# Kernel optimization log

Measured on AMD Instinct MI355X. Metric: run time of the kernel, lower is better.

The kernel has to match this reference:

```python
import jax, jax.numpy as jnp
import numpy as np

B, T, D, H = 128, 512, 16, 512


def lstm_layer(x, h0, c0, Wih, Whh, b):
    """Single LSTM layer, batch_first input x: (B,T,Din). Torch gate order i,f,g,o.
    b is the sum of torch's b_ih + b_hh (identical math)."""
    def step(carry, xt):
        h, c = carry
        gates = xt @ Wih.T + h @ Whh.T + b  # (B, 4H)
        i, f, g, o = jnp.split(gates, 4, axis=-1)
        i = jax.nn.sigmoid(i)
        f = jax.nn.sigmoid(f)
        g = jnp.tanh(g)
        o = jax.nn.sigmoid(o)
        c = f * c + i * g
        h = o * jnp.tanh(c)
        return (h, c), h

    (hT, cT), ys = jax.lax.scan(step, (h0, c0), jnp.swapaxes(x, 0, 1))
    return jnp.swapaxes(ys, 0, 1), hT, cT  # (B,T,H), (B,H), (B,H)


def setup_inputs() -> dict:
    key = jax.random.key(0)
    ks = jax.random.split(key, 16)
    s = 1.0 / np.sqrt(H)  # torch LSTM/Linear init scale
    u = lambda k, shape: jax.random.uniform(k, shape, jnp.float32, -s, s)
    return {
        "x": jax.random.normal(ks[0], (B, T, D), jnp.float32),
        # encoder layer 0: input_dim -> H ; layer 1: H -> H
        "enc_Wih0": u(ks[1], (4 * H, D)),
        "enc_Whh0": u(ks[2], (4 * H, H)),
        "enc_b0": u(ks[3], (4 * H,)),
        "enc_Wih1": u(ks[4], (4 * H, H)),
        "enc_Whh1": u(ks[5], (4 * H, H)),
        "enc_b1": u(ks[6], (4 * H,)),
        # decoder layers: H -> H
        "dec_Wih0": u(ks[7], (4 * H, H)),
        "dec_Whh0": u(ks[8], (4 * H, H)),
        "dec_b0": u(ks[9], (4 * H,)),
        "dec_Wih1": u(ks[10], (4 * H, H)),
        "dec_Whh1": u(ks[11], (4 * H, H)),
        "dec_b1": u(ks[12], (4 * H,)),
        # output projection H -> D
        "W_out": u(ks[13], (D, H)),
        "b_out": u(ks[14], (D,)),
    }


def reference(x, enc_Wih0, enc_Whh0, enc_b0, enc_Wih1, enc_Whh1, enc_b1,
              dec_Wih0, dec_Whh0, dec_b0, dec_Wih1, dec_Whh1, dec_b1,
              W_out, b_out):
    z = jnp.zeros((x.shape[0], H), x.dtype)
    # encoder (2 stacked layers, eval mode -> no dropout)
    y0, h0, c0 = lstm_layer(x, z, z, enc_Wih0, enc_Whh0, enc_b0)
    y1, h1, c1 = lstm_layer(y0, z, z, enc_Wih1, enc_Whh1, enc_b1)
    encoding = h1  # h_n[-1]
    # decoder input: encoding repeated across time
    dec_in = jnp.broadcast_to(encoding[:, None, :], (x.shape[0], x.shape[1], H))
    # decoder initial state = encoder final (h_n, c_n), per-layer
    d0, _, _ = lstm_layer(dec_in, h0, c0, dec_Wih0, dec_Whh0, dec_b0)
    d1, _, _ = lstm_layer(d0, h1, c1, dec_Wih1, dec_Whh1, dec_b1)
    reconstructed = d1 @ W_out.T + b_out  # (B,T,D)
    return reconstructed, encoding
```

## Files before the change

kernel.cpp:

```cpp
#include <hip/hip_runtime.h>
#include <math.h>


#define NB 128
#define NT 512
#define ND 16
#define NH 512
#define NWG 256
#define NTHR 256
#define NGRP 8
#define GWG 32

typedef __attribute__((ext_vector_type(8))) short short8;
typedef __attribute__((ext_vector_type(4))) float float4v;
typedef __attribute__((ext_vector_type(4))) unsigned int uint4v;

#define SCOPE_AGT __HIP_MEMORY_SCOPE_AGENT
#define SCOPE_WG  __HIP_MEMORY_SCOPE_WORKGROUP

#define BAR_BYTES 16384
#define PLANE_BYTES (NB * NH * 4)
#define CHUNK_BYTES (32 * NB * 4)
#define AH_PLANE(wsB, L, par) ((wsB) + BAR_BYTES + (size_t)((L) * 2 + (par)) * PLANE_BYTES)
#define H3F_PTR(wsB, par) ((float*)((wsB) + BAR_BYTES + 8 * (size_t)PLANE_BYTES + (size_t)(par) * NB * NH * 4))

__device__ __forceinline__ void st_u32_agt(unsigned* p, unsigned v) {
  __hip_atomic_store(p, v, __ATOMIC_RELAXED, SCOPE_AGT);
}
__device__ __forceinline__ unsigned ld_u32_agt(const unsigned* p) {
  return __hip_atomic_load(p, __ATOMIC_RELAXED, SCOPE_AGT);
}
__device__ __forceinline__ unsigned long long ld_u64_agt(const void* p) {
  return __hip_atomic_load((const unsigned long long*)p, __ATOMIC_RELAXED, SCOPE_AGT);
}

__device__ __forceinline__ void loadpair(bool fast, const char* pa, const char* pb,
                                         uint4v (&d)[4]) {
  if (fast) {
    asm volatile(
        "global_load_dwordx4 %0, %4, off sc0\n\t"
        "global_load_dwordx4 %1, %4, off offset:16 sc0\n\t"
        "global_load_dwordx4 %2, %5, off sc0\n\t"
        "global_load_dwordx4 %3, %5, off offset:16 sc0\n\t"
        "s_waitcnt vmcnt(0)"
        : "=&v"(d[0]), "=&v"(d[1]), "=&v"(d[2]), "=&v"(d[3])
        : "v"(pa), "v"(pb)
        : "memory");
  } else {
#pragma unroll
    for (int r = 0; r < 2; ++r) {
      const char* base = r ? pb : pa;
      unsigned long long q0 = ld_u64_agt(base);
      unsigned long long q1 = ld_u64_agt(base + 8);
      unsigned long long q2 = ld_u64_agt(base + 16);
      unsigned long long q3 = ld_u64_agt(base + 24);
      d[2 * r][0] = (unsigned)q0; d[2 * r][1] = (unsigned)(q0 >> 32);
      d[2 * r][2] = (unsigned)q1; d[2 * r][3] = (unsigned)(q1 >> 32);
      d[2 * r + 1][0] = (unsigned)q2; d[2 * r + 1][1] = (unsigned)(q2 >> 32);
      d[2 * r + 1][2] = (unsigned)q3; d[2 * r + 1][3] = (unsigned)(q3 >> 32);
    }
  }
}

__device__ __forceinline__ void gbar(unsigned* flags, int hb, unsigned& epoch) {
  ++epoch;
  __syncthreads();
  if (threadIdx.x < 64) {
    if (threadIdx.x == 0) st_u32_agt(flags + hb, epoch);
    const unsigned* fp = flags + (threadIdx.x & 31);
    for (;;) {
      unsigned v = ld_u32_agt(fp);
      if (__all((int)(v - epoch) >= 0)) break;
      __builtin_amdgcn_s_sleep(1);
    }
  }
  __syncthreads();
}

__device__ __forceinline__ unsigned short f2bf(float f) {
  union { float f; unsigned u; } v; v.f = f;
  unsigned r = v.u + 0x7fffu + ((v.u >> 16) & 1u);
  return (unsigned short)(r >> 16);
}
__device__ __forceinline__ float bf2f(unsigned short u) {
  union { float f; unsigned u; } v; v.u = ((unsigned)u) << 16; return v.f;
}
__device__ __forceinline__ void split2(float f, unsigned short& hi, unsigned short& lo) {
  hi = f2bf(f);
  lo = f2bf(f - bf2f(hi));
}
__device__ __forceinline__ void load_wfrag(const float* __restrict__ p, short8& h, short8& l) {
#pragma unroll
  for (int j = 0; j < 8; ++j) {
    unsigned short a, b2; split2(p[j], a, b2);
    h[j] = (short)a; l[j] = (short)b2;
  }
}
__device__ __forceinline__ void load_frags_single(const float* __restrict__ W, int w, int hb, int lane,
                                                  short8 (&fh)[4][4], short8 (&fl)[4][4]) {
  const int ln = lane & 15, lq = lane >> 4;
#pragma unroll
  for (int cc = 0; cc < 4; ++cc) {
    const int k = (w * 4 + cc) * 32 + lq * 8;
#pragma unroll
    for (int g = 0; g < 4; ++g)
      load_wfrag(W + (size_t)(g * NH + hb * 16 + ln) * NH + k, fh[cc][g], fl[cc][g]);
  }
}
__device__ __forceinline__ void load_frags_concat(const float* __restrict__ Wa, const float* __restrict__ Wb,
                                                  int w, int hb, int lane,
                                                  short8 (&fh)[8][4], short8 (&fl)[8][4]) {
  const int ln = lane & 15, lq = lane >> 4;
#pragma unroll
  for (int cc = 0; cc < 8; ++cc) {
    const int k = (w * 8 + cc) * 32 + lq * 8;
    const float* W = (k < 512) ? Wa : Wb;
    const int kk = (k < 512) ? k : k - 512;
#pragma unroll
    for (int g = 0; g < 4; ++g)
      load_wfrag(W + (size_t)(g * NH + hb * 16 + ln) * NH + kk, fh[cc][g], fl[cc][g]);
  }
}

__device__ __forceinline__ void consume2(const uint4v& a, const uint4v& b,
                                         const short8 (&wh)[4], const short8 (&wl)[4],
                                         float4v (&acc)[4]) {
  unsigned x0 = a[0], x1 = a[1], x2 = a[2], x3 = a[3];
  unsigned x4 = b[0], x5 = b[1], x6 = b[2], x7 = b[3];
  union U { unsigned u[4]; short8 s; } A, L;
  A.u[0] = (x0 & 0xffffu) | (x1 << 16);
  A.u[1] = (x2 & 0xffffu) | (x3 << 16);
  A.u[2] = (x4 & 0xffffu) | (x5 << 16);
  A.u[3] = (x6 & 0xffffu) | (x7 << 16);
  L.u[0] = (x0 >> 16) | (x1 & 0xffff0000u);
  L.u[1] = (x2 >> 16) | (x3 & 0xffff0000u);
  L.u[2] = (x4 >> 16) | (x5 & 0xffff0000u);
  L.u[3] = (x6 >> 16) | (x7 & 0xffff0000u);
  const short8 ah = A.s, al = L.s;
#pragma unroll
  for (int g = 0; g < 4; ++g) {
    acc[g] = __builtin_amdgcn_mfma_f32_16x16x32_bf16(ah, wh[g], acc[g], 0, 0, 0);
    acc[g] = __builtin_amdgcn_mfma_f32_16x16x32_bf16(ah, wl[g], acc[g], 0, 0, 0);
    acc[g] = __builtin_amdgcn_mfma_f32_16x16x32_bf16(al, wh[g], acc[g], 0, 0, 0);
  }
}
__device__ __forceinline__ void write_red(float* __restrict__ red, int w, int lane, const float4v (&acc)[4]) {
  const int ln = lane & 15, lq = lane >> 4;
#pragma unroll
  for (int g = 0; g < 4; ++g)
#pragma unroll
    for (int r = 0; r < 4; ++r)
      red[((w * 4 + g) * 16 + (lq * 4 + r)) * 16 + ln] = acc[g][r];
}
__device__ __forceinline__ void store_h(bool fast, char* __restrict__ plane, int b, int hid, float h) {
  unsigned short hi, lo; split2(h, hi, lo);
  const size_t off = (size_t)(hid >> 5) * CHUNK_BYTES + (size_t)b * 128 + (size_t)(hid & 31) * 4;
  unsigned* p = (unsigned*)(plane + off);
  unsigned v = (unsigned)hi | ((unsigned)lo << 16);
  if (fast) __hip_atomic_store(p, v, __ATOMIC_RELAXED, SCOPE_WG);
  else      st_u32_agt(p, v);
}
__device__ __forceinline__ void st_f32s(bool fast, float* p, float v) {
  if (fast) __hip_atomic_store(p, v, __ATOMIC_RELAXED, SCOPE_WG);
  else      __hip_atomic_store(p, v, __ATOMIC_RELAXED, SCOPE_AGT);
}
__device__ __forceinline__ float sigf(float v) { return 1.f / (1.f + __expf(-v)); }

extern "C" __global__ __launch_bounds__(NTHR, 1)
void lstm_ae_kernel(const float* __restrict__ x,
                    const float* __restrict__ eWih0, const float* __restrict__ eWhh0, const float* __restrict__ eb0,
                    const float* __restrict__ eWih1, const float* __restrict__ eWhh1, const float* __restrict__ eb1,
                    const float* __restrict__ dWih0, const float* __restrict__ dWhh0, const float* __restrict__ db0,
                    const float* __restrict__ dWih1, const float* __restrict__ dWhh1, const float* __restrict__ db1,
                    const float* __restrict__ Wout,  const float* __restrict__ bout,
                    float* __restrict__ out, char* __restrict__ wsB) {
  __shared__ float red0[4 * 4 * 16 * 16];
  __shared__ float red1[4 * 4 * 16 * 16];
  __shared__ unsigned sh_slot;

  unsigned* xcnt   = (unsigned*)(wsB + 9216);
  unsigned* gflags = (unsigned*)(wsB + 10240);

  const int tid = threadIdx.x;
  const int lane = tid & 63;
  const int w = tid >> 6;

  const unsigned xcc = (unsigned)__builtin_amdgcn_s_getreg(63508) & 15u;
  if (tid == 0)
    sh_slot = __hip_atomic_fetch_add(xcnt + (xcc & 7u), 1u, __ATOMIC_RELAXED, SCOPE_AGT);
  __syncthreads();
  const unsigned slot = sh_slot;
  if (tid == 0) st_u32_agt(gflags + blockIdx.x, 1u);
  if (tid < 64) {
    for (;;) {
      int ok = 1;
#pragma unroll
      for (int j = 0; j < 4; ++j) ok &= (ld_u32_agt(gflags + lane * 4 + j) != 0u);
      if (__all(ok)) break;
      __builtin_amdgcn_s_sleep(1);
    }
  }
  __syncthreads();
  bool good = (slot < GWG);
#pragma unroll
  for (int k = 0; k < 8; ++k) good = good && (ld_u32_agt(xcnt + k) == GWG);

  const int grp = good ? (int)(xcc & 7u) : (blockIdx.x & 7);
  const int hb  = good ? (int)slot        : (blockIdx.x >> 3);
  const bool fast = good;

  unsigned* flags = (unsigned*)(wsB + (size_t)grp * 1024);
  unsigned epoch = 0;

  const int b0 = grp * 16;
  const int ln = lane & 15, lq = lane >> 4;
  const int aoff = (b0 + ln) * 128 + lq * 32;
  const int bi = tid >> 4, hi_ = tid & 15;
  const int b = b0 + bi, hid = hb * 16 + hi_;
  const float4v zacc = {0.f, 0.f, 0.f, 0.f};

  store_h(fast, AH_PLANE(wsB, 0, 1), b, hid, 0.f);
  store_h(fast, AH_PLANE(wsB, 1, 1), b, hid, 0.f);
  float c0 = 0.f, c1 = 0.f, c2 = 0.f, c3 = 0.f;
  const float eb0v[4] = {eb0[hid], eb0[NH + hid], eb0[2 * NH + hid], eb0[3 * NH + hid]};
  const float eb1v[4] = {eb1[hid], eb1[NH + hid], eb1[2 * NH + hid], eb1[3 * NH + hid]};
  const float db1v[4] = {db1[hid], db1[NH + hid], db1[2 * NH + hid], db1[3 * NH + hid]};

  short8 w0h[4][4], w0l[4][4];
  short8 w1h[8][4], w1l[8][4];
  load_frags_single(eWhh0, w, hb, lane, w0h, w0l);
  load_frags_concat(eWih1, eWhh1, w, hb, lane, w1h, w1l);
  gbar(flags, hb, epoch);

  float h0fin = 0.f, h1fin = 0.f;

  for (int i = 0; i <= NT; ++i) {
    const int pw = i & 1, pr = pw ^ 1;
    const int te = i - 1;
    const int pA = te & 1, pB = pA ^ 1;
    const char* p0 = AH_PLANE(wsB, 0, pr);
    const char* p1 = (w < 2) ? AH_PLANE(wsB, 0, pA) : AH_PLANE(wsB, 1, pB);
    const int c1i = (w < 2) ? w * 8 : (w - 2) * 8;
    float4v acc0[4] = {zacc, zacc, zacc, zacc};
    float4v acc1[4] = {zacc, zacc, zacc, zacc};
    uint4v d[4];

    loadpair(fast, p0 + (size_t)(w * 4 + 0) * CHUNK_BYTES + aoff,
                   p0 + (size_t)(w * 4 + 1) * CHUNK_BYTES + aoff, d);
    consume2(d[0], d[1], w0h[0], w0l[0], acc0);
    consume2(d[2], d[3], w0h[1], w0l[1], acc0);
    loadpair(fast, p0 + (size_t)(w * 4 + 2) * CHUNK_BYTES + aoff,
                   p0 + (size_t)(w * 4 + 3) * CHUNK_BYTES + aoff, d);
    consume2(d[0], d[1], w0h[2], w0l[2], acc0);
    consume2(d[2], d[3], w0h[3], w0l[3], acc0);
    write_red(red0, w, lane, acc0);
#pragma unroll
    for (int pp = 0; pp < 4; ++pp) {
      loadpair(fast, p1 + (size_t)(c1i + 2 * pp) * CHUNK_BYTES + aoff,
                     p1 + (size_t)(c1i + 2 * pp + 1) * CHUNK_BYTES + aoff, d);
      consume2(d[0], d[1], w1h[2 * pp], w1l[2 * pp], acc1);
      consume2(d[2], d[3], w1h[2 * pp + 1], w1l[2 * pp + 1], acc1);
    }
    write_red(red1, w, lane, acc1);
    __syncthreads();

    if (i < NT) {
      float s[4];
#pragma unroll
      for (int g = 0; g < 4; ++g) {
        float v = eb0v[g];
#pragma unroll
        for (int ww = 0; ww < 4; ++ww) v += red0[((ww * 4 + g) * 16 + bi) * 16 + hi_];
        s[g] = v;
      }
      const float* xr = x + ((size_t)b * NT + i) * ND;
      float xv[16];
#pragma unroll
      for (int j = 0; j < 16; ++j) xv[j] = xr[j];
#pragma unroll
      for (int g = 0; g < 4; ++g) {
        const float* wr = eWih0 + (size_t)(g * NH + hid) * ND;
        float v = 0.f;
#pragma unroll
        for (int j = 0; j < 16; ++j) v += xv[j] * wr[j];
        s[g] += v;
      }
      float ig = sigf(s[0]), fg = sigf(s[1]), gg = tanhf(s[2]), og = sigf(s[3]);
      c0 = fg * c0 + ig * gg;
      float h = og * tanhf(c0);
      store_h(fast, AH_PLANE(wsB, 0, pw), b, hid, h);
      if (i == NT - 1) h0fin = h;
    }
    if (i >= 1) {
      float s[4];
#pragma unroll
      for (int g = 0; g < 4; ++g) {
        float v = eb1v[g];
#pragma unroll
        for (int ww = 0; ww < 4; ++ww) v += red1[((ww * 4 + g) * 16 + bi) * 16 + hi_];
        s[g] = v;
      }
      float ig = sigf(s[0]), fg = sigf(s[1]), gg = tanhf(s[2]), og = sigf(s[3]);
      c1 = fg * c1 + ig * gg;
      float h = og * tanhf(c1);
      store_h(fast, AH_PLANE(wsB, 1, pA), b, hid, h);
      if (te == NT - 1) h1fin = h;
    }
    gbar(flags, hb, epoch);
  }

  out[(size_t)NB * NT * ND + (size_t)b * NH + hid] = h1fin;
  c2 = c0; c3 = c1;
  store_h(fast, AH_PLANE(wsB, 2, 1), b, hid, h0fin);
  store_h(fast, AH_PLANE(wsB, 3, 1), b, hid, h1fin);

  float Gbreg[4];
  load_frags_single(dWih0, w, hb, lane, w0h, w0l);
  {
    const char* ph = AH_PLANE(wsB, 1, 1);
    float4v acc[4] = {zacc, zacc, zacc, zacc};
    uint4v d[4];
    loadpair(fast, ph + (size_t)(w * 4 + 0) * CHUNK_BYTES + aoff,
                   ph + (size_t)(w * 4 + 1) * CHUNK_BYTES + aoff, d);
    consume2(d[0], d[1], w0h[0], w0l[0], acc);
    consume2(d[2], d[3], w0h[1], w0l[1], acc);
    loadpair(fast, ph + (size_t)(w * 4 + 2) * CHUNK_BYTES + aoff,
                   ph + (size_t)(w * 4 + 3) * CHUNK_BYTES + aoff, d);
    consume2(d[0], d[1], w0h[2], w0l[2], acc);
    consume2(d[2], d[3], w0h[3], w0l[3], acc);
    write_red(red0, w, lane, acc);
    __syncthreads();
#pragma unroll
    for (int g = 0; g < 4; ++g) {
      float v = db0[g * NH + hid];
#pragma unroll
      for (int ww = 0; ww < 4; ++ww) v += red0[((ww * 4 + g) * 16 + bi) * 16 + hi_];
      Gbreg[g] = v;
    }
  }
  load_frags_single(dWhh0, w, hb, lane, w0h, w0l);
  load_frags_concat(dWih1, dWhh1, w, hb, lane, w1h, w1l);
  gbar(flags, hb, epoch);

  const int idxA = hb * 8 + w * 2, idxB = idxA + 1;
  const int pbA = b0 + (idxA >> 4), pdA = idxA & 15;
  const int pbB = b0 + (idxB >> 4), pdB = idxB & 15;

  for (int i = 0; i <= NT + 1; ++i) {
    const int pw = i & 1, pr = pw ^ 1;
    const int te = i - 1, tp = i - 2;
    const int pA = te & 1, pB = pA ^ 1;
    const char* p0 = AH_PLANE(wsB, 2, pr);
    const char* p1 = (w < 2) ? AH_PLANE(wsB, 2, pA) : AH_PLANE(wsB, 3, pB);
    const int c1i = (w < 2) ? w * 8 : (w - 2) * 8;
    const float* H3 = H3F_PTR(wsB, tp & 1);
    float4v acc0[4] = {zacc, zacc, zacc, zacc};
    float4v acc1[4] = {zacc, zacc, zacc, zacc};
    uint4v d[4];

    loadpair(fast, p0 + (size_t)(w * 4 + 0) * CHUNK_BYTES + aoff,
                   p0 + (size_t)(w * 4 + 1) * CHUNK_BYTES + aoff, d);
    consume2(d[0], d[1], w0h[0], w0l[0], acc0);
    consume2(d[2], d[3], w0h[1], w0l[1], acc0);
    loadpair(fast, p0 + (size_t)(w * 4 + 2) * CHUNK_BYTES + aoff,
                   p0 + (size_t)(w * 4 + 3) * CHUNK_BYTES + aoff, d);
    consume2(d[0], d[1], w0h[2], w0l[2], acc0);
    consume2(d[2], d[3], w0h[3], w0l[3], acc0);
    write_red(red0, w, lane, acc0);
#pragma unroll
    for (int pp = 0; pp < 4; ++pp) {
      loadpair(fast, p1 + (size_t)(c1i + 2 * pp) * CHUNK_BYTES + aoff,
                     p1 + (size_t)(c1i + 2 * pp + 1) * CHUNK_BYTES + aoff, d);
      consume2(d[0], d[1], w1h[2 * pp], w1l[2 * pp], acc1);
      consume2(d[2], d[3], w1h[2 * pp + 1], w1l[2 * pp + 1], acc1);
    }
    write_red(red1, w, lane, acc1);
    uint4v dp[4];
    loadpair(fast, (const char*)(H3 + (size_t)pbA * NH) + (size_t)lane * 32,
                   (const char*)(H3 + (size_t)pbB * NH) + (size_t)lane * 32, dp);
    __syncthreads();

    if (i >= 2) {
#pragma unroll
      for (int rep = 0; rep < 2; ++rep) {
        union PU { uint4v u; float f[4]; } u0, u1;
        u0.u = dp[2 * rep]; u1.u = dp[2 * rep + 1];
        const int pd = rep ? pdB : pdA;
        const float* wr = Wout + (size_t)pd * NH + lane * 8;
        float ssum = u0.f[0] * wr[0] + u0.f[1] * wr[1] + u0.f[2] * wr[2] + u0.f[3] * wr[3]
                   + u1.f[0] * wr[4] + u1.f[1] * wr[5] + u1.f[2] * wr[6] + u1.f[3] * wr[7];
#pragma unroll
        for (int off = 32; off >= 1; off >>= 1) ssum += __shfl_xor(ssum, off, 64);
        if (lane == 0)
          out[((size_t)(rep ? pbB : pbA) * NT + tp) * ND + pd] = ssum + bout[pd];
      }
    }
    if (i < NT) {
      float s[4];
#pragma unroll
      for (int g = 0; g < 4; ++g) {
        float v = Gbreg[g];
#pragma unroll
        for (int ww = 0; ww < 4; ++ww) v += red0[((ww * 4 + g) * 16 + bi) * 16 + hi_];
        s[g] = v;
      }
      float ig = sigf(s[0]), fg = sigf(s[1]), gg = tanhf(s[2]), og = sigf(s[3]);
      c2 = fg * c2 + ig * gg;
      float h = og * tanhf(c2);
      store_h(fast, AH_PLANE(wsB, 2, pw), b, hid, h);
    }
    if (i >= 1 && i <= NT) {
      float s[4];
#pragma unroll
      for (int g = 0; g < 4; ++g) {
        float v = db1v[g];
#pragma unroll
        for (int ww = 0; ww < 4; ++ww) v += red1[((ww * 4 + g) * 16 + bi) * 16 + hi_];
        s[g] = v;
      }
      float ig = sigf(s[0]), fg = sigf(s[1]), gg = tanhf(s[2]), og = sigf(s[3]);
      c3 = fg * c3 + ig * gg;
      float h = og * tanhf(c3);
      store_h(fast, AH_PLANE(wsB, 3, pA), b, hid, h);
      st_f32s(fast, H3F_PTR(wsB, pA) + (size_t)b * NH + hid, h);
    }
    if (i != NT + 1) gbar(flags, hb, epoch);
  }
}

extern "C" void kernel_launch(void* const* d_in, const int* in_sizes, int n_in,
                              void* d_out, int out_size, void* d_ws, size_t ws_size,
                              hipStream_t stream) {
  const float* xp    = (const float*)d_in[0];
  const float* eWih0 = (const float*)d_in[1];
  const float* eWhh0 = (const float*)d_in[2];
  const float* eb0   = (const float*)d_in[3];
  const float* eWih1 = (const float*)d_in[4];
  const float* eWhh1 = (const float*)d_in[5];
  const float* eb1   = (const float*)d_in[6];
  const float* dWih0 = (const float*)d_in[7];
  const float* dWhh0 = (const float*)d_in[8];
  const float* db0   = (const float*)d_in[9];
  const float* dWih1 = (const float*)d_in[10];
  const float* dWhh1 = (const float*)d_in[11];
  const float* db1   = (const float*)d_in[12];
  const float* Wout  = (const float*)d_in[13];
  const float* bout  = (const float*)d_in[14];

  hipMemsetAsync(d_ws, 0, BAR_BYTES, stream);
  lstm_ae_kernel<<<NWG, NTHR, 0, stream>>>(
      xp, eWih0, eWhh0, eb0, eWih1, eWhh1, eb1,
      dWih0, dWhh0, db0, dWih1, dWhh1, db1, Wout, bout,
      (float*)d_out, (char*)d_ws);
}
```

Before: 9.032 ms.

## Drop XCC-aware group placement and use uniform agent-scope loads/stores

Measured after the change: 9.218 ms. 1.02x slower.

```diff
diff --git a/kernel.cpp b/kernel.cpp
--- a/kernel.cpp
+++ b/kernel.cpp
@@ -16,7 +16,6 @@
 typedef __attribute__((ext_vector_type(4))) unsigned int uint4v;
 
 #define SCOPE_AGT __HIP_MEMORY_SCOPE_AGENT
-#define SCOPE_WG  __HIP_MEMORY_SCOPE_WORKGROUP
 
 #define BAR_BYTES 16384
 #define PLANE_BYTES (NB * NH * 4)
@@ -30,36 +29,18 @@
 __device__ __forceinline__ unsigned ld_u32_agt(const unsigned* p) {
   return __hip_atomic_load(p, __ATOMIC_RELAXED, SCOPE_AGT);
 }
-__device__ __forceinline__ unsigned long long ld_u64_agt(const void* p) {
-  return __hip_atomic_load((const unsigned long long*)p, __ATOMIC_RELAXED, SCOPE_AGT);
-}
-
-__device__ __forceinline__ void loadpair(bool fast, const char* pa, const char* pb,
+
+__device__ __forceinline__ void loadpair(const char* pa, const char* pb,
                                          uint4v (&d)[4]) {
-  if (fast) {
-    asm volatile(
-        "global_load_dwordx4 %0, %4, off sc0\n\t"
-        "global_load_dwordx4 %1, %4, off offset:16 sc0\n\t"
-        "global_load_dwordx4 %2, %5, off sc0\n\t"
-        "global_load_dwordx4 %3, %5, off offset:16 sc0\n\t"
-        "s_waitcnt vmcnt(0)"
-        : "=&v"(d[0]), "=&v"(d[1]), "=&v"(d[2]), "=&v"(d[3])
-        : "v"(pa), "v"(pb)
-        : "memory");
-  } else {
-#pragma unroll
-    for (int r = 0; r < 2; ++r) {
-      const char* base = r ? pb : pa;
-      unsigned long long q0 = ld_u64_agt(base);
-      unsigned long long q1 = ld_u64_agt(base + 8);
-      unsigned long long q2 = ld_u64_agt(base + 16);
-      unsigned long long q3 = ld_u64_agt(base + 24);
-      d[2 * r][0] = (unsigned)q0; d[2 * r][1] = (unsigned)(q0 >> 32);
-      d[2 * r][2] = (unsigned)q1; d[2 * r][3] = (unsigned)(q1 >> 32);
-      d[2 * r + 1][0] = (unsigned)q2; d[2 * r + 1][1] = (unsigned)(q2 >> 32);
-      d[2 * r + 1][2] = (unsigned)q3; d[2 * r + 1][3] = (unsigned)(q3 >> 32);
-    }
-  }
+  asm volatile(
+      "global_load_dwordx4 %0, %4, off sc1\n\t"
+      "global_load_dwordx4 %1, %4, off offset:16 sc1\n\t"
+      "global_load_dwordx4 %2, %5, off sc1\n\t"
+      "global_load_dwordx4 %3, %5, off offset:16 sc1\n\t"
+      "s_waitcnt vmcnt(0)"
+      : "=&v"(d[0]), "=&v"(d[1]), "=&v"(d[2]), "=&v"(d[3])
+      : "v"(pa), "v"(pb)
+      : "memory");
 }
 
 __device__ __forceinline__ void gbar(unsigned* flags, int hb, unsigned& epoch) {
@@ -152,17 +133,11 @@
     for (int r = 0; r < 4; ++r)
       red[((w * 4 + g) * 16 + (lq * 4 + r)) * 16 + ln] = acc[g][r];
 }
-__device__ __forceinline__ void store_h(bool fast, char* __restrict__ plane, int b, int hid, float h) {
+__device__ __forceinline__ void store_h(char* __restrict__ plane, int b, int hid, float h) {
   unsigned short hi, lo; split2(h, hi, lo);
   const size_t off = (size_t)(hid >> 5) * CHUNK_BYTES + (size_t)b * 128 + (size_t)(hid & 31) * 4;
-  unsigned* p = (unsigned*)(plane + off);
   unsigned v = (unsigned)hi | ((unsigned)lo << 16);
-  if (fast) __hip_atomic_store(p, v, __ATOMIC_RELAXED, SCOPE_WG);
-  else      st_u32_agt(p, v);
-}
-__device__ __forceinline__ void st_f32s(bool fast, float* p, float v) {
-  if (fast) __hip_atomic_store(p, v, __ATOMIC_RELAXED, SCOPE_WG);
-  else      __hip_atomic_store(p, v, __ATOMIC_RELAXED, SCOPE_AGT);
+  st_u32_agt((unsigned*)(plane + off), v);
 }
 __device__ __forceinline__ float sigf(float v) { return 1.f / (1.f + __expf(-v)); }
 
@@ -176,38 +151,13 @@
                     float* __restrict__ out, char* __restrict__ wsB) {
   __shared__ float red0[4 * 4 * 16 * 16];
   __shared__ float red1[4 * 4 * 16 * 16];
-  __shared__ unsigned sh_slot;
-
-  unsigned* xcnt   = (unsigned*)(wsB + 9216);
-  unsigned* gflags = (unsigned*)(wsB + 10240);
 
   const int tid = threadIdx.x;
   const int lane = tid & 63;
   const int w = tid >> 6;
 
-  const unsigned xcc = (unsigned)__builtin_amdgcn_s_getreg(63508) & 15u;
-  if (tid == 0)
-    sh_slot = __hip_atomic_fetch_add(xcnt + (xcc & 7u), 1u, __ATOMIC_RELAXED, SCOPE_AGT);
-  __syncthreads();
-  const unsigned slot = sh_slot;
-  if (tid == 0) st_u32_agt(gflags + blockIdx.x, 1u);
-  if (tid < 64) {
-    for (;;) {
-      int ok = 1;
-#pragma unroll
-      for (int j = 0; j < 4; ++j) ok &= (ld_u32_agt(gflags + lane * 4 + j) != 0u);
-      if (__all(ok)) break;
-      __builtin_amdgcn_s_sleep(1);
-    }
-  }
-  __syncthreads();
-  bool good = (slot < GWG);
-#pragma unroll
-  for (int k = 0; k < 8; ++k) good = good && (ld_u32_agt(xcnt + k) == GWG);
-
-  const int grp = good ? (int)(xcc & 7u) : (blockIdx.x & 7);
-  const int hb  = good ? (int)slot        : (blockIdx.x >> 3);
-  const bool fast = good;
+  const int grp = (int)(blockIdx.x & 7u);
+  const int hb  = (int)(blockIdx.x >> 3);
 
   unsigned* flags = (unsigned*)(wsB + (size_t)grp * 1024);
   unsigned epoch = 0;
@@ -219,8 +169,8 @@
   const int b = b0 + bi, hid = hb * 16 + hi_;
   const float4v zacc = {0.f, 0.f, 0.f, 0.f};
 
-  store_h(fast, AH_PLANE(wsB, 0, 1), b, hid, 0.f);
-  store_h(fast, AH_PLANE(wsB, 1, 1), b, hid, 0.f);
+  store_h(AH_PLANE(wsB, 0, 1), b, hid, 0.f);
+  store_h(AH_PLANE(wsB, 1, 1), b, hid, 0.f);
   float c0 = 0.f, c1 = 0.f, c2 = 0.f, c3 = 0.f;
   const float eb0v[4] = {eb0[hid], eb0[NH + hid], eb0[2 * NH + hid], eb0[3 * NH + hid]};
   const float eb1v[4] = {eb1[hid], eb1[NH + hid], eb1[2 * NH + hid], eb1[3 * NH + hid]};
@@ -245,19 +195,19 @@
     float4v acc1[4] = {zacc, zacc, zacc, zacc};
     uint4v d[4];
 
-    loadpair(fast, p0 + (size_t)(w * 4 + 0) * CHUNK_BYTES + aoff,
-                   p0 + (size_t)(w * 4 + 1) * CHUNK_BYTES + aoff, d);
+    loadpair(p0 + (size_t)(w * 4 + 0) * CHUNK_BYTES + aoff,
+             p0 + (size_t)(w * 4 + 1) * CHUNK_BYTES + aoff, d);
     consume2(d[0], d[1], w0h[0], w0l[0], acc0);
     consume2(d[2], d[3], w0h[1], w0l[1], acc0);
-    loadpair(fast, p0 + (size_t)(w * 4 + 2) * CHUNK_BYTES + aoff,
-                   p0 + (size_t)(w * 4 + 3) * CHUNK_BYTES + aoff, d);
+    loadpair(p0 + (size_t)(w * 4 + 2) * CHUNK_BYTES + aoff,
+             p0 + (size_t)(w * 4 + 3) * CHUNK_BYTES + aoff, d);
     consume2(d[0], d[1], w0h[2], w0l[2], acc0);
     consume2(d[2], d[3], w0h[3], w0l[3], acc0);
     write_red(red0, w, lane, acc0);
 #pragma unroll
     for (int pp = 0; pp < 4; ++pp) {
-      loadpair(fast, p1 + (size_t)(c1i + 2 * pp) * CHUNK_BYTES + aoff,
-                     p1 + (size_t)(c1i + 2 * pp + 1) * CHUNK_BYTES + aoff, d);
+      loadpair(p1 + (size_t)(c1i + 2 * pp) * CHUNK_BYTES + aoff,
+               p1 + (size_t)(c1i + 2 * pp + 1) * CHUNK_BYTES + aoff, d);
       consume2(d[0], d[1], w1h[2 * pp], w1l[2 * pp], acc1);
       consume2(d[2], d[3], w1h[2 * pp + 1], w1l[2 * pp + 1], acc1);
     }
@@ -288,7 +238,7 @@
       float ig = sigf(s[0]), fg = sigf(s[1]), gg = tanhf(s[2]), og = sigf(s[3]);
       c0 = fg * c0 + ig * gg;
       float h = og * tanhf(c0);
-      store_h(fast, AH_PLANE(wsB, 0, pw), b, hid, h);
+      store_h(AH_PLANE(wsB, 0, pw), b, hid, h);
       if (i == NT - 1) h0fin = h;
     }
     if (i >= 1) {
@@ -303,7 +253,7 @@
       float ig = sigf(s[0]), fg = sigf(s[1]), gg = tanhf(s[2]), og = sigf(s[3]);
       c1 = fg * c1 + ig * gg;
       float h = og * tanhf(c1);
-      store_h(fast, AH_PLANE(wsB, 1, pA), b, hid, h);
+      store_h(AH_PLANE(wsB, 1, pA), b, hid, h);
       if (te == NT - 1) h1fin = h;
     }
     gbar(flags, hb, epoch);
@@ -311,8 +261,8 @@
 
   out[(size_t)NB * NT * ND + (size_t)b * NH + hid] = h1fin;
   c2 = c0; c3 = c1;
-  store_h(fast, AH_PLANE(wsB, 2, 1), b, hid, h0fin);
-  store_h(fast, AH_PLANE(wsB, 3, 1), b, hid, h1fin);
+  store_h(AH_PLANE(wsB, 2, 1), b, hid, h0fin);
+  store_h(AH_PLANE(wsB, 3, 1), b, hid, h1fin);
 
   float Gbreg[4];
   load_frags_single(dWih0, w, hb, lane, w0h, w0l);
@@ -320,12 +270,12 @@
     const char* ph = AH_PLANE(wsB, 1, 1);
     float4v acc[4] = {zacc, zacc, zacc, zacc};
     uint4v d[4];
-    loadpair(fast, ph + (size_t)(w * 4 + 0) * CHUNK_BYTES + aoff,
-                   ph + (size_t)(w * 4 + 1) * CHUNK_BYTES + aoff, d);
+    loadpair(ph + (size_t)(w * 4 + 0) * CHUNK_BYTES + aoff,
+             ph + (size_t)(w * 4 + 1) * CHUNK_BYTES + aoff, d);
     consume2(d[0], d[1], w0h[0], w0l[0], acc);
     consume2(d[2], d[3], w0h[1], w0l[1], acc);
-    loadpair(fast, ph + (size_t)(w * 4 + 2) * CHUNK_BYTES + aoff,
-                   ph + (size_t)(w * 4 + 3) * CHUNK_BYTES + aoff, d);
+    loadpair(ph + (size_t)(w * 4 + 2) * CHUNK_BYTES + aoff,
+             ph + (size_t)(w * 4 + 3) * CHUNK_BYTES + aoff, d);
     consume2(d[0], d[1], w0h[2], w0l[2], acc);
     consume2(d[2], d[3], w0h[3], w0l[3], acc);
     write_red(red0, w, lane, acc);
@@ -358,26 +308,26 @@
     float4v acc1[4] = {zacc, zacc, zacc, zacc};
     uint4v d[4];
 
-    loadpair(fast, p0 + (size_t)(w * 4 + 0) * CHUNK_BYTES + aoff,
-                   p0 + (size_t)(w * 4 + 1) * CHUNK_BYTES + aoff, d);
+    loadpair(p0 + (size_t)(w * 4 + 0) * CHUNK_BYTES + aoff,
+             p0 + (size_t)(w * 4 + 1) * CHUNK_BYTES + aoff, d);
     consume2(d[0], d[1], w0h[0], w0l[0], acc0);
     consume2(d[2], d[3], w0h[1], w0l[1], acc0);
-    loadpair(fast, p0 + (size_t)(w * 4 + 2) * CHUNK_BYTES + aoff,
-                   p0 + (size_t)(w * 4 + 3) * CHUNK_BYTES + aoff, d);
+    loadpair(p0 + (size_t)(w * 4 + 2) * CHUNK_BYTES + aoff,
+             p0 + (size_t)(w * 4 + 3) * CHUNK_BYTES + aoff, d);
     consume2(d[0], d[1], w0h[2], w0l[2], acc0);
     consume2(d[2], d[3], w0h[3], w0l[3], acc0);
     write_red(red0, w, lane, acc0);
 #pragma unroll
     for (int pp = 0; pp < 4; ++pp) {
-      loadpair(fast, p1 + (size_t)(c1i + 2 * pp) * CHUNK_BYTES + aoff,
-                     p1 + (size_t)(c1i + 2 * pp + 1) * CHUNK_BYTES + aoff, d);
+      loadpair(p1 + (size_t)(c1i + 2 * pp) * CHUNK_BYTES + aoff,
+               p1 + (size_t)(c1i + 2 * pp + 1) * CHUNK_BYTES + aoff, d);
       consume2(d[0], d[1], w1h[2 * pp], w1l[2 * pp], acc1);
       consume2(d[2], d[3], w1h[2 * pp + 1], w1l[2 * pp + 1], acc1);
     }
     write_red(red1, w, lane, acc1);
     uint4v dp[4];
-    loadpair(fast, (const char*)(H3 + (size_t)pbA * NH) + (size_t)lane * 32,
-                   (const char*)(H3 + (size_t)pbB * NH) + (size_t)lane * 32, dp);
+    loadpair((const char*)(H3 + (size_t)pbA * NH) + (size_t)lane * 32,
+             (const char*)(H3 + (size_t)pbB * NH) + (size_t)lane * 32, dp);
     __syncthreads();
 
     if (i >= 2) {
@@ -407,7 +357,7 @@
       float ig = sigf(s[0]), fg = sigf(s[1]), gg = tanhf(s[2]), og = sigf(s[3]);
       c2 = fg * c2 + ig * gg;
       float h = og * tanhf(c2);
-      store_h(fast, AH_PLANE(wsB, 2, pw), b, hid, h);
+      store_h(AH_PLANE(wsB, 2, pw), b, hid, h);
     }
     if (i >= 1 && i <= NT) {
       float s[4];
@@ -421,8 +371,9 @@
       float ig = sigf(s[0]), fg = sigf(s[1]), gg = tanhf(s[2]), og = sigf(s[3]);
       c3 = fg * c3 + ig * gg;
       float h = og * tanhf(c3);
-      store_h(fast, AH_PLANE(wsB, 3, pA), b, hid, h);
-      st_f32s(fast, H3F_PTR(wsB, pA) + (size_t)b * NH + hid, h);
+      store_h(AH_PLANE(wsB, 3, pA), b, hid, h);
+      __hip_atomic_store(H3F_PTR(wsB, pA) + (size_t)b * NH + hid, h,
+                         __ATOMIC_RELAXED, SCOPE_AGT);
     }
     if (i != NT + 1) gbar(flags, hb, epoch);
   }
```

## Double workgroup to eight waves, splitting the K reduction across more waves

Applied to the files above, without the earlier changes.

Result: slower. 22.82 ms (+152.7%).

```diff
diff --git a/kernel.cpp b/kernel.cpp
--- a/kernel.cpp
+++ b/kernel.cpp
@@ -7,7 +7,8 @@
 #define ND 16
 #define NH 512
 #define NWG 256
-#define NTHR 256
+#define NTHR 512
+#define NWAVE 8
 #define NGRP 8
 #define GWG 32
 
@@ -97,23 +98,23 @@
   }
 }
 __device__ __forceinline__ void load_frags_single(const float* __restrict__ W, int w, int hb, int lane,
+                                                  short8 (&fh)[2][4], short8 (&fl)[2][4]) {
+  const int ln = lane & 15, lq = lane >> 4;
+#pragma unroll
+  for (int cc = 0; cc < 2; ++cc) {
+    const int k = (w * 2 + cc) * 32 + lq * 8;
+#pragma unroll
+    for (int g = 0; g < 4; ++g)
+      load_wfrag(W + (size_t)(g * NH + hb * 16 + ln) * NH + k, fh[cc][g], fl[cc][g]);
+  }
+}
+__device__ __forceinline__ void load_frags_concat(const float* __restrict__ Wa, const float* __restrict__ Wb,
+                                                  int w, int hb, int lane,
                                                   short8 (&fh)[4][4], short8 (&fl)[4][4]) {
   const int ln = lane & 15, lq = lane >> 4;
 #pragma unroll
   for (int cc = 0; cc < 4; ++cc) {
     const int k = (w * 4 + cc) * 32 + lq * 8;
-#pragma unroll
-    for (int g = 0; g < 4; ++g)
-      load_wfrag(W + (size_t)(g * NH + hb * 16 + ln) * NH + k, fh[cc][g], fl[cc][g]);
-  }
-}
-__device__ __forceinline__ void load_frags_concat(const float* __restrict__ Wa, const float* __restrict__ Wb,
-                                                  int w, int hb, int lane,
-                                                  short8 (&fh)[8][4], short8 (&fl)[8][4]) {
-  const int ln = lane & 15, lq = lane >> 4;
-#pragma unroll
-  for (int cc = 0; cc < 8; ++cc) {
-    const int k = (w * 8 + cc) * 32 + lq * 8;
     const float* W = (k < 512) ? Wa : Wb;
     const int kk = (k < 512) ? k : k - 512;
 #pragma unroll
@@ -174,8 +175,8 @@
                     const float* __restrict__ dWih1, const float* __restrict__ dWhh1, const float* __restrict__ db1,
                     const float* __restrict__ Wout,  const float* __restrict__ bout,
                     float* __restrict__ out, char* __restrict__ wsB) {
-  __shared__ float red0[4 * 4 * 16 * 16];
-  __shared__ float red1[4 * 4 * 16 * 16];
+  __shared__ float red0[NWAVE * 4 * 16 * 16];
+  __shared__ float red1[NWAVE * 4 * 16 * 16];
   __shared__ unsigned sh_slot;
 
   unsigned* xcnt   = (unsigned*)(wsB + 9216);
@@ -184,6 +185,7 @@
   const int tid = threadIdx.x;
   const int lane = tid & 63;
   const int w = tid >> 6;
+  const bool act = (tid < 256);
 
   const unsigned xcc = (unsigned)__builtin_amdgcn_s_getreg(63508) & 15u;
   if (tid == 0)
@@ -216,18 +218,20 @@
   const int ln = lane & 15, lq = lane >> 4;
   const int aoff = (b0 + ln) * 128 + lq * 32;
   const int bi = tid >> 4, hi_ = tid & 15;
-  const int b = b0 + bi, hid = hb * 16 + hi_;
+  const int b = b0 + (bi & 15), hid = hb * 16 + hi_;
   const float4v zacc = {0.f, 0.f, 0.f, 0.f};
 
-  store_h(fast, AH_PLANE(wsB, 0, 1), b, hid, 0.f);
-  store_h(fast, AH_PLANE(wsB, 1, 1), b, hid, 0.f);
+  if (act) {
+    store_h(fast, AH_PLANE(wsB, 0, 1), b, hid, 0.f);
+    store_h(fast, AH_PLANE(wsB, 1, 1), b, hid, 0.f);
+  }
   float c0 = 0.f, c1 = 0.f, c2 = 0.f, c3 = 0.f;
   const float eb0v[4] = {eb0[hid], eb0[NH + hid], eb0[2 * NH + hid], eb0[3 * NH + hid]};
   const float eb1v[4] = {eb1[hid], eb1[NH + hid], eb1[2 * NH + hid], eb1[3 * NH + hid]};
   const float db1v[4] = {db1[hid], db1[NH + hid], db1[2 * NH + hid], db1[3 * NH + hid]};
 
-  short8 w0h[4][4], w0l[4][4];
-  short8 w1h[8][4], w1l[8][4];
+  short8 w0h[2][4], w0l[2][4];
+  short8 w1h[4][4], w1l[4][4];
   load_frags_single(eWhh0, w, hb, lane, w0h, w0l);
   load_frags_concat(eWih1, eWhh1, w, hb, lane, w1h, w1l);
   gbar(flags, hb, epoch);
@@ -239,23 +243,19 @@
     const int te = i - 1;
     const int pA = te & 1, pB = pA ^ 1;
     const char* p0 = AH_PLANE(wsB, 0, pr);
-    const char* p1 = (w < 2) ? AH_PLANE(wsB, 0, pA) : AH_PLANE(wsB, 1, pB);
-    const int c1i = (w < 2) ? w * 8 : (w - 2) * 8;
+    const char* p1 = (w < 4) ? AH_PLANE(wsB, 0, pA) : AH_PLANE(wsB, 1, pB);
+    const int c1i = (w < 4) ? w * 4 : (w - 4) * 4;
     float4v acc0[4] = {zacc, zacc, zacc, zacc};
     float4v acc1[4] = {zacc, zacc, zacc, zacc};
     uint4v d[4];
 
-    loadpair(fast, p0 + (size_t)(w * 4 + 0) * CHUNK_BYTES + aoff,
-                   p0 + (size_t)(w * 4 + 1) * CHUNK_BYTES + aoff, d);
+    loadpair(fast, p0 + (size_t)(w * 2 + 0) * CHUNK_BYTES + aoff,
+                   p0 + (size_t)(w * 2 + 1) * CHUNK_BYTES + aoff, d);
     consume2(d[0], d[1], w0h[0], w0l[0], acc0);
     consume2(d[2], d[3], w0h[1], w0l[1], acc0);
-    loadpair(fast, p0 + (size_t)(w * 4 + 2) * CHUNK_BYTES + aoff,
-                   p0 + (size_t)(w * 4 + 3) * CHUNK_BYTES + aoff, d);
-    consume2(d[0], d[1], w0h[2], w0l[2], acc0);
-    consume2(d[2], d[3], w0h[3], w0l[3], acc0);
     write_red(red0, w, lane, acc0);
 #pragma unroll
-    for (int pp = 0; pp < 4; ++pp) {
+    for (int pp = 0; pp < 2; ++pp) {
       loadpair(fast, p1 + (size_t)(c1i + 2 * pp) * CHUNK_BYTES + aoff,
                      p1 + (size_t)(c1i + 2 * pp + 1) * CHUNK_BYTES + aoff, d);
       consume2(d[0], d[1], w1h[2 * pp], w1l[2 * pp], acc1);
@@ -264,13 +264,13 @@
     write_red(red1, w, lane, acc1);
     __syncthreads();
 
-    if (i < NT) {
+    if (act && i < NT) {
       float s[4];
 #pragma unroll
       for (int g = 0; g < 4; ++g) {
         float v = eb0v[g];
 #pragma unroll
-        for (int ww = 0; ww < 4; ++ww) v += red0[((ww * 4 + g) * 16 + bi) * 16 + hi_];
+        for (int ww = 0; ww < NWAVE; ++ww) v += red0[((ww * 4 + g) * 16 + bi) * 16 + hi_];
         s[g] = v;
       }
       const float* xr = x + ((size_t)b * NT + i) * ND;
@@ -291,13 +291,13 @@
       store_h(fast, AH_PLANE(wsB, 0, pw), b, hid, h);
       if (i == NT - 1) h0fin = h;
     }
-    if (i >= 1) {
+    if (act && i >= 1) {
       float s[4];
 #pragma unroll
       for (int g = 0; g < 4; ++g) {
         float v = eb1v[g];
 #pragma unroll
-        for (int ww = 0; ww < 4; ++ww) v += red1[((ww * 4 + g) * 16 + bi) * 16 + hi_];
+        for (int ww = 0; ww < NWAVE; ++ww) v += red1[((ww * 4 + g) * 16 + bi) * 16 + hi_];
         s[g] = v;
       }
       float ig = sigf(s[0]), fg = sigf(s[1]), gg = tanhf(s[2]), og = sigf(s[3]);
@@ -309,10 +309,12 @@
     gbar(flags, hb, epoch);
   }
 
-  out[(size_t)NB * NT * ND + (size_t)b * NH + hid] = h1fin;
+  if (act) {
+    out[(size_t)NB * NT * ND + (size_t)b * NH + hid] = h1fin;
+    store_h(fast, AH_PLANE(wsB, 2, 1), b, hid, h0fin);
+    store_h(fast, AH_PLANE(wsB, 3, 1), b, hid, h1fin);
+  }
   c2 = c0; c3 = c1;
-  store_h(fast, AH_PLANE(wsB, 2, 1), b, hid, h0fin);
-  store_h(fast, AH_PLANE(wsB, 3, 1), b, hid, h1fin);
 
   float Gbreg[4];
   load_frags_single(dWih0, w, hb, lane, w0h, w0l);
@@ -320,21 +322,17 @@
     const char* ph = AH_PLANE(wsB, 1, 1);
     float4v acc[4] = {zacc, zacc, zacc, zacc};
     uint4v d[4];
-    loadpair(fast, ph + (size_t)(w * 4 + 0) * CHUNK_BYTES + aoff,
-                   ph + (size_t)(w * 4 + 1) * CHUNK_BYTES + aoff, d);
+    loadpair(fast, ph + (size_t)(w * 2 + 0) * CHUNK_BYTES + aoff,
+                   ph + (size_t)(w * 2 + 1) * CHUNK_BYTES + aoff, d);
     consume2(d[0], d[1], w0h[0], w0l[0], acc);
     consume2(d[2], d[3], w0h[1], w0l[1], acc);
-    loadpair(fast, ph + (size_t)(w * 4 + 2) * CHUNK_BYTES + aoff,
-                   ph + (size_t)(w * 4 + 3) * CHUNK_BYTES + aoff, d);
-    consume2(d[0], d[1], w0h[2], w0l[2], acc);
-    consume2(d[2], d[3], w0h[3], w0l[3], acc);
     write_red(red0, w, lane, acc);
     __syncthreads();
 #pragma unroll
     for (int g = 0; g < 4; ++g) {
       float v = db0[g * NH + hid];
 #pragma unroll
-      for (int ww = 0; ww < 4; ++ww) v += red0[((ww * 4 + g) * 16 + bi) * 16 + hi_];
+      for (int ww = 0; ww < NWAVE; ++ww) v += red0[((ww * 4 + g) * 16 + bi) * 16 + hi_];
       Gbreg[g] = v;
     }
   }
@@ -343,32 +341,28 @@
   gbar(flags, hb, epoch);
 
   const int idxA = hb * 8 + w * 2, idxB = idxA + 1;
-  const int pbA = b0 + (idxA >> 4), pdA = idxA & 15;
-  const int pbB = b0 + (idxB >> 4), pdB = idxB & 15;
+  const int pbA = b0 + ((idxA >> 4) & 15), pdA = idxA & 15;
+  const int pbB = b0 + ((idxB >> 4) & 15), pdB = idxB & 15;
 
   for (int i = 0; i <= NT + 1; ++i) {
     const int pw = i & 1, pr = pw ^ 1;
     const int te = i - 1, tp = i - 2;
     const int pA = te & 1, pB = pA ^ 1;
     const char* p0 = AH_PLANE(wsB, 2, pr);
-    const char* p1 = (w < 2) ? AH_PLANE(wsB, 2, pA) : AH_PLANE(wsB, 3, pB);
-    const int c1i = (w < 2) ? w * 8 : (w - 2) * 8;
+    const char* p1 = (w < 4) ? AH_PLANE(wsB, 2, pA) : AH_PLANE(wsB, 3, pB);
+    const int c1i = (w < 4) ? w * 4 : (w - 4) * 4;
     const float* H3 = H3F_PTR(wsB, tp & 1);
     float4v acc0[4] = {zacc, zacc, zacc, zacc};
     float4v acc1[4] = {zacc, zacc, zacc, zacc};
     uint4v d[4];
 
-    loadpair(fast, p0 + (size_t)(w * 4 + 0) * CHUNK_BYTES + aoff,
-                   p0 + (size_t)(w * 4 + 1) * CHUNK_BYTES + aoff, d);
+    loadpair(fast, p0 + (size_t)(w * 2 + 0) * CHUNK_BYTES + aoff,
+                   p0 + (size_t)(w * 2 + 1) * CHUNK_BYTES + aoff, d);
     consume2(d[0], d[1], w0h[0], w0l[0], acc0);
     consume2(d[2], d[3], w0h[1], w0l[1], acc0);
-    loadpair(fast, p0 + (size_t)(w * 4 + 2) * CHUNK_BYTES + aoff,
-                   p0 + (size_t)(w * 4 + 3) * CHUNK_BYTES + aoff, d);
-    consume2(d[0], d[1], w0h[2], w0l[2], acc0);
-    consume2(d[2], d[3], w0h[3], w0l[3], acc0);
     write_red(red0, w, lane, acc0);
 #pragma unroll
-    for (int pp = 0; pp < 4; ++pp) {
+    for (int pp = 0; pp < 2; ++pp) {
       loadpair(fast, p1 + (size_t)(c1i + 2 * pp) * CHUNK_BYTES + aoff,
                      p1 + (size_t)(c1i + 2 * pp + 1) * CHUNK_BYTES + aoff, d);
       consume2(d[0], d[1], w1h[2 * pp], w1l[2 * pp], acc1);
@@ -376,11 +370,12 @@
     }
     write_red(red1, w, lane, acc1);
     uint4v dp[4];
-    loadpair(fast, (const char*)(H3 + (size_t)pbA * NH) + (size_t)lane * 32,
-                   (const char*)(H3 + (size_t)pbB * NH) + (size_t)lane * 32, dp);
+    if (w < 4)
+      loadpair(fast, (const char*)(H3 + (size_t)pbA * NH) + (size_t)lane * 32,
+                     (const char*)(H3 + (size_t)pbB * NH) + (size_t)lane * 32, dp);
     __syncthreads();
 
-    if (i >= 2) {
+    if (w < 4 && i >= 2) {
 #pragma unroll
       for (int rep = 0; rep < 2; ++rep) {
         union PU { uint4v u; float f[4]; } u0, u1;
@@ -395,13 +390,13 @@
           out[((size_t)(rep ? pbB : pbA) * NT + tp) * ND + pd] = ssum + bout[pd];
       }
     }
-    if (i < NT) {
+    if (act && i < NT) {
       float s[4];
 #pragma unroll
       for (int g = 0; g < 4; ++g) {
         float v = Gbreg[g];
 #pragma unroll
-        for (int ww = 0; ww < 4; ++ww) v += red0[((ww * 4 + g) * 16 + bi) * 16 + hi_];
+        for (int ww = 0; ww < NWAVE; ++ww) v += red0[((ww * 4 + g) * 16 + bi) * 16 + hi_];
         s[g] = v;
       }
       float ig = sigf(s[0]), fg = sigf(s[1]), gg = tanhf(s[2]), og = sigf(s[3]);
@@ -409,13 +404,13 @@
       float h = og * tanhf(c2);
       store_h(fast, AH_PLANE(wsB, 2, pw), b, hid, h);
     }
-    if (i >= 1 && i <= NT) {
+    if (act && i >= 1 && i <= NT) {
       float s[4];
 #pragma unroll
       for (int g = 0; g < 4; ++g) {
         float v = db1v[g];
 #pragma unroll
-        for (int ww = 0; ww < 4; ++ww) v += red1[((ww * 4 + g) * 16 + bi) * 16 + hi_];
+        for (int ww = 0; ww < NWAVE; ++ww) v += red1[((ww * 4 + g) * 16 + bi) * 16 + hi_];
         s[g] = v;
       }
       float ig = sigf(s[0]), fg = sigf(s[1]), gg = tanhf(s[2]), og = sigf(s[3]);
```
